# Kernel tuning notes

Measured on AMD Instinct MI355X. Metric: run time of the kernel, lower is better.

Reference implementation:

```python
import jax, jax.numpy as jnp
import numpy as np

BLOCK = 32  # GGUF Q8_0 block size


def setup_inputs() -> dict:
    key = jax.random.key(0)
    k1, k2, k3, k4 = jax.random.split(key, 4)
    O, I = 11008, 4096
    x = jax.random.normal(k1, (32, I), dtype=jnp.float32)
    qweight = jax.random.randint(k2, (O, I), 0, 255, dtype=jnp.int32)
    scales = jax.random.uniform(k3, (O, I // BLOCK), dtype=jnp.float32) * 0.01
    bias = jax.random.normal(k4, (O,), dtype=jnp.float32)
    return {"x": x, "qweight": qweight, "scales": scales, "bias": bias}


def dequantize(qweight, scales):
    # Q8_0-style: signed int8 quants, one fp scale per block of 32 along in-dim.
    O, I = qweight.shape
    q = (qweight.astype(scales.dtype) - 127.0).reshape(O, I // BLOCK, BLOCK)
    w = q * scales[:, :, None]  # [O, nb, BLOCK]
    return w.reshape(O, I)


def reference(x, qweight, scales, bias):
    # On-the-fly dequant fused with F.linear: y = x @ W^T + b
    w = dequantize(qweight, scales)           # [O, I]
    return jnp.einsum('bi,oi->bo', x, w) + bias
```

## Files before the change

### kernel.cpp

```cpp
#include <hip/hip_runtime.h>
#include <hip/hip_bf16.h>


#define O_DIM  11008
#define I_DIM  4096
#define NB     128
#define B_DIM  32
#define NSPLIT 16
#define KT     (I_DIM / NSPLIT)
#define PART_STRIDE (B_DIM * O_DIM)

typedef __attribute__((ext_vector_type(8))) short bf16x8;
typedef __attribute__((ext_vector_type(4))) float f32x4;

static __device__ __forceinline__ unsigned short f2bf(float f) {
    return __builtin_bit_cast(unsigned short, __float2bfloat16(f));
}

static __device__ __forceinline__ bf16x8 dequant8(const int4 qa, const int4 qb,
                                                  const float s) {
    const float c = -127.0f * s;
    bf16x8 v;
    v[0] = (short)f2bf(fmaf((float)qa.x, s, c));
    v[1] = (short)f2bf(fmaf((float)qa.y, s, c));
    v[2] = (short)f2bf(fmaf((float)qa.z, s, c));
    v[3] = (short)f2bf(fmaf((float)qa.w, s, c));
    v[4] = (short)f2bf(fmaf((float)qb.x, s, c));
    v[5] = (short)f2bf(fmaf((float)qb.y, s, c));
    v[6] = (short)f2bf(fmaf((float)qb.z, s, c));
    v[7] = (short)f2bf(fmaf((float)qb.w, s, c));
    return v;
}

__global__ __launch_bounds__(256) void gemm_kernel(const float* __restrict__ x,
                                                   const int*   __restrict__ qw,
                                                   const float* __restrict__ scales,
                                                   float*       __restrict__ part) {
    __shared__ unsigned short x_s[B_DIM * KT];

    const int t    = threadIdx.x;
    const int wav  = t >> 6;
    const int lan  = t & 63;
    const int lrow = lan & 15;
    const int lq   = lan >> 4;

    const int split  = blockIdx.x;
    const int k_base = split * KT;
    const int o_row  = blockIdx.y * 64 + wav * 16 + lrow;

    {
        const int m  = t >> 3;
        const int k0 = (t & 7) * 32;
        const float4* xv = reinterpret_cast<const float4*>(x + m * I_DIM + k_base + k0);
#pragma unroll
        for (int j = 0; j < 4; ++j) {
            const float4 va = xv[2 * j];
            const float4 vb = xv[2 * j + 1];
            bf16x8 v;
            v[0] = (short)f2bf(va.x); v[1] = (short)f2bf(va.y);
            v[2] = (short)f2bf(va.z); v[3] = (short)f2bf(va.w);
            v[4] = (short)f2bf(vb.x); v[5] = (short)f2bf(vb.y);
            v[6] = (short)f2bf(vb.z); v[7] = (short)f2bf(vb.w);
            const int addr = ((m * KT + k0 + j * 8) * 2) ^ ((m & 7) << 4);
            *reinterpret_cast<bf16x8*>(reinterpret_cast<char*>(x_s) + addr) = v;
        }
    }

    const int* __restrict__ wq = qw + o_row * I_DIM + k_base + lq * 8;

    float sc[8];
    {
        const float4* sp = reinterpret_cast<const float4*>(&scales[o_row * NB + split * 8]);
        const float4 s0 = sp[0], s1 = sp[1];
        sc[0] = s0.x; sc[1] = s0.y; sc[2] = s0.z; sc[3] = s0.w;
        sc[4] = s1.x; sc[5] = s1.y; sc[6] = s1.z; sc[7] = s1.w;
    }

    int4 wa0, wb0, wc0, wd0, wa1, wb1, wc1, wd1, wa2, wb2, wc2, wd2;

#define LOADW(A, B, C, D, c) {                         \
        const int* wp = wq + (c) * 64;                 \
        A = *reinterpret_cast<const int4*>(wp);        \
        B = *reinterpret_cast<const int4*>(wp + 4);    \
        C = *reinterpret_cast<const int4*>(wp + 32);   \
        D = *reinterpret_cast<const int4*>(wp + 36); }

    LOADW(wa0, wb0, wc0, wd0, 0)
    LOADW(wa1, wb1, wc1, wd1, 1)

    __syncthreads();

    f32x4 acc0 = {0.f, 0.f, 0.f, 0.f};
    f32x4 acc1 = {0.f, 0.f, 0.f, 0.f};
    const int swz = (lrow & 7) << 4;

#define CONSUME(A, B, C, D, c) {                                                              \
        const int kb = (c) * 64 + lq * 8;                                                     \
        const bf16x8 a0 = *reinterpret_cast<const bf16x8*>(                                   \
            reinterpret_cast<const char*>(x_s) + ((( lrow       * KT + kb) * 2) ^ swz));      \
        const bf16x8 a1 = *reinterpret_cast<const bf16x8*>(                                   \
            reinterpret_cast<const char*>(x_s) + ((((lrow + 16) * KT + kb) * 2) ^ swz));      \
        const bf16x8 bA = dequant8(A, B, sc[2 * (c)]);                                        \
        acc0 = __builtin_amdgcn_mfma_f32_16x16x32_bf16(a0, bA, acc0, 0, 0, 0);                \
        acc1 = __builtin_amdgcn_mfma_f32_16x16x32_bf16(a1, bA, acc1, 0, 0, 0);                \
        const bf16x8 a2 = *reinterpret_cast<const bf16x8*>(                                   \
            reinterpret_cast<const char*>(x_s) + ((( lrow       * KT + kb + 32) * 2) ^ swz)); \
        const bf16x8 a3 = *reinterpret_cast<const bf16x8*>(                                   \
            reinterpret_cast<const char*>(x_s) + ((((lrow + 16) * KT + kb + 32) * 2) ^ swz)); \
        const bf16x8 bB = dequant8(C, D, sc[2 * (c) + 1]);                                    \
        acc0 = __builtin_amdgcn_mfma_f32_16x16x32_bf16(a2, bB, acc0, 0, 0, 0);                \
        acc1 = __builtin_amdgcn_mfma_f32_16x16x32_bf16(a3, bB, acc1, 0, 0, 0); }

    LOADW(wa2, wb2, wc2, wd2, 2)
    CONSUME(wa0, wb0, wc0, wd0, 0)
    LOADW(wa0, wb0, wc0, wd0, 3)
    CONSUME(wa1, wb1, wc1, wd1, 1)
    CONSUME(wa2, wb2, wc2, wd2, 2)
    CONSUME(wa0, wb0, wc0, wd0, 3)

#undef LOADW
#undef CONSUME

    float* pp = part + split * PART_STRIDE;
#pragma unroll
    for (int r = 0; r < 4; ++r) {
        const int m = lq * 4 + r;
        pp[m * O_DIM + o_row]        = acc0[r];
        pp[(m + 16) * O_DIM + o_row] = acc1[r];
    }
}

__global__ __launch_bounds__(256) void reduce_kernel(const float* __restrict__ part,
                                                     const float* __restrict__ bias,
                                                     float* __restrict__ out) {
    const int o = blockIdx.x * 256 + threadIdx.x;
    const int m = blockIdx.y;
    float v = bias[o];
#pragma unroll
    for (int s = 0; s < NSPLIT; ++s)
        v += part[s * PART_STRIDE + m * O_DIM + o];
    out[m * O_DIM + o] = v;
}

extern "C" void kernel_launch(void* const* d_in, const int* in_sizes, int n_in,
                              void* d_out, int out_size, void* d_ws, size_t ws_size,
                              hipStream_t stream) {
    const float* x      = (const float*)d_in[0];
    const int*   qw     = (const int*)d_in[1];
    const float* scales = (const float*)d_in[2];
    const float* bias   = (const float*)d_in[3];
    float*       out    = (float*)d_out;
    float*       part   = (float*)d_ws;

    hipLaunchKernelGGL(gemm_kernel, dim3(NSPLIT, O_DIM / 64), dim3(256), 0, stream,
                       x, qw, scales, part);

    hipLaunchKernelGGL(reduce_kernel, dim3(O_DIM / 256, B_DIM), dim3(256), 0, stream,
                       part, bias, out);
}
```

Measured before the change: 47.14 us.

## Halve split-K count, deepen weight pipeline, vectorize reduction with nontemporal accesses

Reduces the K-split from 16 to 8, so each block covers 512 K-elements with an extended 8-stage rolling weight-load pipeline, and issues the weight loads before staging x into LDS. This halves the partial-sum traffic written by the GEMM and read back by the reduce kernel. The reduce kernel now uses float4 vector loads and stores with nontemporal hints, and the partial stores are nontemporal. The trade-offs are a larger LDS footprint (32 KB per block), fewer blocks, and a launch_bounds occupancy hint of 3 that may limit registers.

```diff
diff --git a/kernel.cpp b/kernel.cpp
--- a/kernel.cpp
+++ b/kernel.cpp
@@ -6,36 +6,37 @@
 #define I_DIM  4096
 #define NB     128
 #define B_DIM  32
-#define NSPLIT 16
+#define NSPLIT 8
 #define KT     (I_DIM / NSPLIT)
 #define PART_STRIDE (B_DIM * O_DIM)
 
 typedef __attribute__((ext_vector_type(8))) short bf16x8;
 typedef __attribute__((ext_vector_type(4))) float f32x4;
+typedef __attribute__((ext_vector_type(4))) int   i32x4;
 
 static __device__ __forceinline__ unsigned short f2bf(float f) {
     return __builtin_bit_cast(unsigned short, __float2bfloat16(f));
 }
 
-static __device__ __forceinline__ bf16x8 dequant8(const int4 qa, const int4 qb,
+static __device__ __forceinline__ bf16x8 dequant8(const i32x4 qa, const i32x4 qb,
                                                   const float s) {
     const float c = -127.0f * s;
     bf16x8 v;
-    v[0] = (short)f2bf(fmaf((float)qa.x, s, c));
-    v[1] = (short)f2bf(fmaf((float)qa.y, s, c));
-    v[2] = (short)f2bf(fmaf((float)qa.z, s, c));
-    v[3] = (short)f2bf(fmaf((float)qa.w, s, c));
-    v[4] = (short)f2bf(fmaf((float)qb.x, s, c));
-    v[5] = (short)f2bf(fmaf((float)qb.y, s, c));
-    v[6] = (short)f2bf(fmaf((float)qb.z, s, c));
-    v[7] = (short)f2bf(fmaf((float)qb.w, s, c));
+    v[0] = (short)f2bf(fmaf((float)qa[0], s, c));
+    v[1] = (short)f2bf(fmaf((float)qa[1], s, c));
+    v[2] = (short)f2bf(fmaf((float)qa[2], s, c));
+    v[3] = (short)f2bf(fmaf((float)qa[3], s, c));
+    v[4] = (short)f2bf(fmaf((float)qb[0], s, c));
+    v[5] = (short)f2bf(fmaf((float)qb[1], s, c));
+    v[6] = (short)f2bf(fmaf((float)qb[2], s, c));
+    v[7] = (short)f2bf(fmaf((float)qb[3], s, c));
     return v;
 }
 
-__global__ __launch_bounds__(256) void gemm_kernel(const float* __restrict__ x,
-                                                   const int*   __restrict__ qw,
-                                                   const float* __restrict__ scales,
-                                                   float*       __restrict__ part) {
+__global__ __launch_bounds__(256, 3) void gemm_kernel(const float* __restrict__ x,
+                                                      const int*   __restrict__ qw,
+                                                      const float* __restrict__ scales,
+                                                      float*       __restrict__ part) {
     __shared__ unsigned short x_s[B_DIM * KT];
 
     const int t    = threadIdx.x;
@@ -48,12 +49,37 @@
     const int k_base = split * KT;
     const int o_row  = blockIdx.y * 64 + wav * 16 + lrow;
 
+    const int* __restrict__ wq = qw + o_row * I_DIM + k_base + lq * 8;
+
+    float sc[16];
+    {
+        const float4* sp = reinterpret_cast<const float4*>(&scales[o_row * NB + split * 16]);
+#pragma unroll
+        for (int j = 0; j < 4; ++j) {
+            const float4 v = sp[j];
+            sc[4 * j + 0] = v.x; sc[4 * j + 1] = v.y;
+            sc[4 * j + 2] = v.z; sc[4 * j + 3] = v.w;
+        }
+    }
+
+    i32x4 wa0, wb0, wc0, wd0, wa1, wb1, wc1, wd1, wa2, wb2, wc2, wd2;
+
+#define LOADW(A, B, C, D, c) {                           \
+        const int* wp = wq + (c) * 64;                   \
+        A = *reinterpret_cast<const i32x4*>(wp);         \
+        B = *reinterpret_cast<const i32x4*>(wp + 4);     \
+        C = *reinterpret_cast<const i32x4*>(wp + 32);    \
+        D = *reinterpret_cast<const i32x4*>(wp + 36); }
+
+    LOADW(wa0, wb0, wc0, wd0, 0)
+    LOADW(wa1, wb1, wc1, wd1, 1)
+
     {
         const int m  = t >> 3;
-        const int k0 = (t & 7) * 32;
+        const int k0 = (t & 7) * 64;
         const float4* xv = reinterpret_cast<const float4*>(x + m * I_DIM + k_base + k0);
 #pragma unroll
-        for (int j = 0; j < 4; ++j) {
+        for (int j = 0; j < 8; ++j) {
             const float4 va = xv[2 * j];
             const float4 vb = xv[2 * j + 1];
             bf16x8 v;
@@ -65,28 +91,6 @@
             *reinterpret_cast<bf16x8*>(reinterpret_cast<char*>(x_s) + addr) = v;
         }
     }
-
-    const int* __restrict__ wq = qw + o_row * I_DIM + k_base + lq * 8;
-
-    float sc[8];
-    {
-        const float4* sp = reinterpret_cast<const float4*>(&scales[o_row * NB + split * 8]);
-        const float4 s0 = sp[0], s1 = sp[1];
-        sc[0] = s0.x; sc[1] = s0.y; sc[2] = s0.z; sc[3] = s0.w;
-        sc[4] = s1.x; sc[5] = s1.y; sc[6] = s1.z; sc[7] = s1.w;
-    }
-
-    int4 wa0, wb0, wc0, wd0, wa1, wb1, wc1, wd1, wa2, wb2, wc2, wd2;
-
-#define LOADW(A, B, C, D, c) {                         \
-        const int* wp = wq + (c) * 64;                 \
-        A = *reinterpret_cast<const int4*>(wp);        \
-        B = *reinterpret_cast<const int4*>(wp + 4);    \
-        C = *reinterpret_cast<const int4*>(wp + 32);   \
-        D = *reinterpret_cast<const int4*>(wp + 36); }
-
-    LOADW(wa0, wb0, wc0, wd0, 0)
-    LOADW(wa1, wb1, wc1, wd1, 1)
 
     __syncthreads();
 
@@ -115,8 +119,16 @@
     CONSUME(wa0, wb0, wc0, wd0, 0)
     LOADW(wa0, wb0, wc0, wd0, 3)
     CONSUME(wa1, wb1, wc1, wd1, 1)
+    LOADW(wa1, wb1, wc1, wd1, 4)
     CONSUME(wa2, wb2, wc2, wd2, 2)
+    LOADW(wa2, wb2, wc2, wd2, 5)
     CONSUME(wa0, wb0, wc0, wd0, 3)
+    LOADW(wa0, wb0, wc0, wd0, 6)
+    CONSUME(wa1, wb1, wc1, wd1, 4)
+    LOADW(wa1, wb1, wc1, wd1, 7)
+    CONSUME(wa2, wb2, wc2, wd2, 5)
+    CONSUME(wa0, wb0, wc0, wd0, 6)
+    CONSUME(wa1, wb1, wc1, wd1, 7)
 
 #undef LOADW
 #undef CONSUME
@@ -125,21 +137,26 @@
 #pragma unroll
     for (int r = 0; r < 4; ++r) {
         const int m = lq * 4 + r;
-        pp[m * O_DIM + o_row]        = acc0[r];
-        pp[(m + 16) * O_DIM + o_row] = acc1[r];
+        __builtin_nontemporal_store(acc0[r], &pp[m * O_DIM + o_row]);
+        __builtin_nontemporal_store(acc1[r], &pp[(m + 16) * O_DIM + o_row]);
     }
 }
 
 __global__ __launch_bounds__(256) void reduce_kernel(const float* __restrict__ part,
                                                      const float* __restrict__ bias,
                                                      float* __restrict__ out) {
-    const int o = blockIdx.x * 256 + threadIdx.x;
-    const int m = blockIdx.y;
-    float v = bias[o];
+    const int idx = blockIdx.x * 256 + threadIdx.x;
+    const int m   = idx / (O_DIM / 4);
+    const int o4  = idx - m * (O_DIM / 4);
+
+    f32x4 v = *reinterpret_cast<const f32x4*>(&bias[o4 * 4]);
 #pragma unroll
-    for (int s = 0; s < NSPLIT; ++s)
-        v += part[s * PART_STRIDE + m * O_DIM + o];
-    out[m * O_DIM + o] = v;
+    for (int s = 0; s < NSPLIT; ++s) {
+        const f32x4 p = __builtin_nontemporal_load(
+            reinterpret_cast<const f32x4*>(&part[s * PART_STRIDE + m * O_DIM + o4 * 4]));
+        v[0] += p[0]; v[1] += p[1]; v[2] += p[2]; v[3] += p[3];
+    }
+    *reinterpret_cast<f32x4*>(&out[m * O_DIM + o4 * 4]) = v;
 }
 
 extern "C" void kernel_launch(void* const* d_in, const int* in_sizes, int n_in,
@@ -155,6 +172,6 @@
     hipLaunchKernelGGL(gemm_kernel, dim3(NSPLIT, O_DIM / 64), dim3(256), 0, stream,
                        x, qw, scales, part);
 
-    hipLaunchKernelGGL(reduce_kernel, dim3(O_DIM / 256, B_DIM), dim3(256), 0, stream,
+    hipLaunchKernelGGL(reduce_kernel, dim3((B_DIM * O_DIM / 4) / 256), dim3(256), 0, stream,
                        part, bias, out);
 }
```

New measurement: 50.45 us. 7.0% more time.
